# Performance work log

Measured on AMD Instinct MI355X. Metric: run time of the kernel, lower is better.

## Reference

```python
import jax, jax.numpy as jnp
import numpy as np

D_MODEL = 1024
NUM_HEADS = 16
B, S = 2, 2048


def setup_inputs() -> dict:
    key = jax.random.key(0)
    ks = jax.random.split(key, 11)
    scale = 1.0 / np.sqrt(D_MODEL)
    inp = {
        'q': jax.random.normal(ks[0], (B, S, D_MODEL), jnp.float32),
        'k': jax.random.normal(ks[1], (B, S, D_MODEL), jnp.float32),
        'v': jax.random.normal(ks[2], (B, S, D_MODEL), jnp.float32),
        'w_q': jax.random.normal(ks[3], (D_MODEL, D_MODEL), jnp.float32) * scale,
        'b_q': jax.random.normal(ks[4], (D_MODEL,), jnp.float32) * 0.01,
        'w_k': jax.random.normal(ks[5], (D_MODEL, D_MODEL), jnp.float32) * scale,
        'b_k': jax.random.normal(ks[6], (D_MODEL,), jnp.float32) * 0.01,
        'w_v': jax.random.normal(ks[7], (D_MODEL, D_MODEL), jnp.float32) * scale,
        'b_v': jax.random.normal(ks[8], (D_MODEL,), jnp.float32) * 0.01,
        'w_o': jax.random.normal(ks[9], (D_MODEL, D_MODEL), jnp.float32) * scale,
        'b_o': jax.random.normal(ks[10], (D_MODEL,), jnp.float32) * 0.01,
    }
    return inp


def reference(q, k, v, w_q, b_q, w_k, b_k, w_v, b_v, w_o, b_o):
    Bq, Sq, D = q.shape
    H = NUM_HEADS
    dh = D // H
    # projections (weights stored as [in, out])
    query = q @ w_q + b_q
    key = k @ w_k + b_k
    value = v @ w_v + b_v
    # [B, S, D] -> [B, H, S, dh]
    query = query.reshape(Bq, Sq, H, dh).transpose(0, 2, 1, 3)
    key = key.reshape(Bq, -1, H, dh).transpose(0, 2, 1, 3)
    value = value.reshape(Bq, -1, H, dh).transpose(0, 2, 1, 3)
    # NOTE: original module does NOT scale by 1/sqrt(dh)
    scores = jnp.einsum('bhqd,bhkd->bhqk', query, key)  # [B,H,S,S]
    causal_mask = jnp.triu(jnp.ones((Sq, Sq), dtype=bool), k=1)  # True above diag
    scores = jnp.where(causal_mask[None, None], -jnp.inf, scores)
    attn = jax.nn.softmax(scores, axis=-1)
    data = jnp.einsum('bhqk,bhkd->bhqd', attn, value)  # [B,H,S,dh]
    # FAITHFUL to original bug: transpose(0,1) then view(B, S, -1)
    data = data.transpose(1, 0, 2, 3).reshape(Bq, Sq, -1)  # [H,B,S,dh] -> [B,S,D]
    return data @ w_o + b_o
```

## Files before the change

### kernel.cpp

```cpp
#include <hip/hip_runtime.h>

typedef __fp16 f16;
typedef __fp16 f16x8 __attribute__((ext_vector_type(8)));
typedef __fp16 f16x4 __attribute__((ext_vector_type(4)));
typedef __fp16 f16x2 __attribute__((ext_vector_type(2)));
typedef float f32x4 __attribute__((ext_vector_type(4)));
typedef float f32x16 __attribute__((ext_vector_type(16)));

#define D_MODEL 1024
#define SEQ 2048
#define NH 16
#define MTOT 4096

typedef const __attribute__((address_space(1))) unsigned int* gp1_t;
typedef __attribute__((address_space(3))) unsigned int* lp3_t;

__device__ __forceinline__ void gload_lds16(const void* g, void* l) {
  __builtin_amdgcn_global_load_lds((gp1_t)g, (lp3_t)l, 16, 0, 0);
}

__device__ __forceinline__ int permrow(int r) {
  int bp = r >> 11, u = (r >> 7) & 15, t = r & 127;
  int g16 = (bp << 4) | u;
  return ((((g16 & 1) << 4) | (g16 >> 1)) << 7) + t;
}

__device__ __forceinline__ unsigned int pkrtz(float a, float b) {
  union { f16x2 h; unsigned int u; } z;
  z.h = __builtin_amdgcn_cvt_pkrtz(a, b);
  return z.u;
}

__global__ __launch_bounds__(256) void cvt_all(const float* __restrict__ q,
                                               const float* __restrict__ k,
                                               const float* __restrict__ v,
                                               const float* __restrict__ wq,
                                               const float* __restrict__ wk,
                                               const float* __restrict__ wv,
                                               const float* __restrict__ wo,
                                               f16* __restrict__ qkv16,
                                               f16* __restrict__ wT) {
  __shared__ float tl[64][65];
  int bid = blockIdx.x, tid = threadIdx.x;
  if (bid < 6144) {
    int i = bid * 256 + tid;
    const int NT = (MTOT * D_MODEL) / 8;
    const float* src;
    int t;
    if (i < NT) { src = q; t = i; }
    else if (i < 2 * NT) { src = k; t = i - NT; }
    else { src = v; t = i - 2 * NT; }
    const float4* s4 = (const float4*)src;
    float4 a = s4[2 * t], b = s4[2 * t + 1];
    f16x8 h;
    h[0] = (f16)a.x; h[1] = (f16)a.y; h[2] = (f16)a.z; h[3] = (f16)a.w;
    h[4] = (f16)b.x; h[5] = (f16)b.y; h[6] = (f16)b.z; h[7] = (f16)b.w;
    *(f16x8*)(qkv16 + (size_t)i * 8) = h;
  } else {
    int bb = bid - 6144;
    int mat = bb >> 8, tile = bb & 255;
    int tk = (tile >> 4) << 6, tn = (tile & 15) << 6;
    const float* W = mat == 0 ? wq : mat == 1 ? wk : mat == 2 ? wv : wo;
    int rr = tid >> 4, c4 = (tid & 15) << 2;
#pragma unroll
    for (int it = 0; it < 4; ++it) {
      const float* p = W + (size_t)(tk + it * 16 + rr) * D_MODEL + tn + c4;
      float4 val = *(const float4*)p;
      tl[it * 16 + rr][c4 + 0] = val.x;
      tl[it * 16 + rr][c4 + 1] = val.y;
      tl[it * 16 + rr][c4 + 2] = val.z;
      tl[it * 16 + rr][c4 + 3] = val.w;
    }
    __syncthreads();
    int n = tid & 63, kseg = (tid >> 6) << 4;
    f16x8 lo, hi;
#pragma unroll
    for (int j = 0; j < 8; ++j) lo[j] = (f16)tl[kseg + j][n];
#pragma unroll
    for (int j = 0; j < 8; ++j) hi[j] = (f16)tl[kseg + 8 + j][n];
    f16* d = wT + (size_t)mat * (D_MODEL * D_MODEL) + (size_t)(tn + n) * D_MODEL + tk + kseg;
    *(f16x8*)d = lo;
    *(f16x8*)(d + 8) = hi;
  }
}

#define SLOT_ELEM 16384
__global__ __launch_bounds__(512, 2) void gemm_qkv(const f16* __restrict__ q16,
                                                   const f16* __restrict__ k16,
                                                   const f16* __restrict__ v16,
                                                   const f16* __restrict__ wT,
                                                   const float* __restrict__ bq,
                                                   const float* __restrict__ bk,
                                                   const float* __restrict__ bv,
                                                   f16* __restrict__ Q16,
                                                   f16* __restrict__ K16,
                                                   f16* __restrict__ VT16) {
  extern __shared__ __attribute__((aligned(16))) f16 sm[];
  const int K = D_MODEL, N = D_MODEL;
  const size_t WEL = (size_t)D_MODEL * D_MODEL;
  int z = blockIdx.z;
  const f16* A = z == 0 ? q16 : z == 1 ? k16 : v16;
  const f16* BT = wT + (size_t)z * WEL;
  const float* bias = z == 0 ? bq : z == 1 ? bk : bv;

  int tid = threadIdx.x;
  int w = tid >> 6, lane = tid & 63;
  int g = lane >> 4, c = lane & 15;
  int wr = w >> 2, wc = w & 3;
  int m0 = blockIdx.x * 256, n0 = blockIdx.y * 256;
  f32x4 acc[8][4] = {};

  int sl0 = lane >> 3, s = lane & 7;
  int u = s ^ sl0;
  int rlow = u >> 2, gsl = u & 3;
  const f16* Agp = A + (size_t)(m0 + w * 32 + 2 * sl0 + rlow) * K + gsl * 8;
  const f16* Bgp = BT + (size_t)(n0 + w * 32 + 2 * sl0 + rlow) * K + gsl * 8;

#define STAGE_QKV(tt, bi)                                                    \
  {                                                                          \
    f16* dA = sm + (bi)*SLOT_ELEM + w * 1024;                                \
    f16* dB = dA + 8192;                                                     \
    const f16* sa = Agp + (size_t)(tt)*32;                                   \
    const f16* sb = Bgp + (size_t)(tt)*32;                                   \
    gload_lds16(sa, dA);                                                     \
    gload_lds16(sa + (size_t)16 * K, dA + 512);                              \
    gload_lds16(sb, dB);                                                     \
    gload_lds16(sb + (size_t)16 * K, dB + 512);                              \
  }

  STAGE_QKV(0, 0)
  STAGE_QKV(1, 1)
  STAGE_QKV(2, 2)

  const int NKT = K / 32;
  for (int t = 0; t < NKT; ++t) {
    if (t < NKT - 2) asm volatile("s_waitcnt vmcnt(8)" ::: "memory");
    else if (t == NKT - 2) asm volatile("s_waitcnt vmcnt(4)" ::: "memory");
    else asm volatile("s_waitcnt vmcnt(0)" ::: "memory");
    __builtin_amdgcn_sched_barrier(0);
    __builtin_amdgcn_s_barrier();
    __builtin_amdgcn_sched_barrier(0);
    if (t + 3 < NKT) STAGE_QKV(t + 3, (t + 3) & 3)

    const char* Ac = (const char*)(sm + (t & 3) * SLOT_ELEM);
    const char* Bc = Ac + 16384;
    f16x8 af[8], bf[4];
#pragma unroll
    for (int mi = 0; mi < 8; ++mi) {
      int row = wr * 128 + mi * 16 + c;
      int tb = (row >> 1) * 128 + (((((row & 1) << 2) | g) ^ ((row >> 1) & 7)) << 4);
      af[mi] = *(const f16x8*)(Ac + tb);
    }
#pragma unroll
    for (int ni = 0; ni < 4; ++ni) {
      int row = wc * 64 + ni * 16 + c;
      int tb = (row >> 1) * 128 + (((((row & 1) << 2) | g) ^ ((row >> 1) & 7)) << 4);
      bf[ni] = *(const f16x8*)(Bc + tb);
    }
    asm volatile("s_waitcnt lgkmcnt(0)" ::: "memory");
    __builtin_amdgcn_sched_barrier(0);
    __builtin_amdgcn_s_setprio(1);
#pragma unroll
    for (int mi = 0; mi < 8; ++mi)
#pragma unroll
      for (int ni = 0; ni < 4; ++ni)
        acc[mi][ni] = __builtin_amdgcn_mfma_f32_16x16x32_f16(af[mi], bf[ni], acc[mi][ni], 0, 0, 0);
    __builtin_amdgcn_s_setprio(0);
  }

  int rb = m0 + wr * 128;
  int cb = n0 + wc * 64;
  if (z < 2) {
    f16* O = z == 0 ? Q16 : K16;
#pragma unroll
    for (int m = 0; m < 8; ++m) {
      int row0 = rb + m * 16 + 4 * g;
#pragma unroll
      for (int n = 0; n < 4; ++n) {
        int col = cb + n * 16 + c;
        float bv2 = bias[col];
#pragma unroll
        for (int r = 0; r < 4; ++r) O[(size_t)(row0 + r) * N + col] = (f16)(acc[m][n][r] + bv2);
      }
    }
  } else {
    f16* O = VT16;
#pragma unroll
    for (int m = 0; m < 8; ++m) {
      int s0f = rb + m * 16 + 4 * g;
      int bb = s0f >> 11, ss = s0f & (SEQ - 1);
#pragma unroll
      for (int n = 0; n < 4; ++n) {
        int col = cb + n * 16 + c;
        float bv2 = bias[col];
        f16x4 hv;
#pragma unroll
        for (int r = 0; r < 4; ++r) hv[r] = (f16)(acc[m][n][r] + bv2);
        *(f16x4*)(O + ((size_t)(bb * NH + (col >> 6)) * 64 + (col & 63)) * SEQ + ss) = hv;
      }
    }
  }
}

__global__ __launch_bounds__(256, 2) void gemm_out(const f16* __restrict__ A,
                                                   const f16* __restrict__ BT,
                                                   const float* __restrict__ bias,
                                                   float* __restrict__ O) {
  const int K = D_MODEL, N = D_MODEL;
  __shared__ f16 As[64 * 64];
  __shared__ f16 Bs[128 * 64];
  int tid = threadIdx.x;
  int w = tid >> 6, lane = tid & 63;
  int g = lane >> 4, c = lane & 15;
  int wr = w >> 1, wc = w & 1;
  int m0 = blockIdx.x * 64, n0 = blockIdx.y * 128;
  f32x4 acc[2][4] = {};

  for (int kt = 0; kt < K; kt += 64) {
#pragma unroll
    for (int i = 0; i < 2; ++i) {
      int seg = w * 2 + i;
      int p = seg * 1024 + lane * 16;
      int row = p >> 7;
      int colb = (p & 127) ^ ((row & 7) << 4);
      int ae = kt + (colb >> 1);
      gload_lds16(A + (size_t)permrow(m0 + row) * K + ae, &As[seg * 512]);
    }
#pragma unroll
    for (int i = 0; i < 4; ++i) {
      int seg = w * 4 + i;
      int p = seg * 1024 + lane * 16;
      int row = p >> 7;
      int colb = (p & 127) ^ ((row & 7) << 4);
      int ae = kt + (colb >> 1);
      gload_lds16(BT + (size_t)(n0 + row) * K + ae, &Bs[seg * 512]);
    }
    __syncthreads();
    f16x8 af[2][2], bf[4][2];
#pragma unroll
    for (int m = 0; m < 2; ++m) {
#pragma unroll
      for (int kk = 0; kk < 2; ++kk) {
        int row = wr * 32 + m * 16 + c;
        int tb = (row * 128 + kk * 64 + g * 16) ^ ((row & 7) << 4);
        af[m][kk] = *(const f16x8*)((const char*)As + tb);
      }
    }
#pragma unroll
    for (int n = 0; n < 4; ++n) {
#pragma unroll
      for (int kk = 0; kk < 2; ++kk) {
        int row = wc * 64 + n * 16 + c;
        int tb = (row * 128 + kk * 64 + g * 16) ^ ((row & 7) << 4);
        bf[n][kk] = *(const f16x8*)((const char*)Bs + tb);
      }
    }
    __builtin_amdgcn_s_setprio(1);
#pragma unroll
    for (int m = 0; m < 2; ++m)
#pragma unroll
      for (int n = 0; n < 4; ++n)
#pragma unroll
        for (int kk = 0; kk < 2; ++kk)
          acc[m][n] = __builtin_amdgcn_mfma_f32_16x16x32_f16(af[m][kk], bf[n][kk], acc[m][n], 0, 0, 0);
    __builtin_amdgcn_s_setprio(0);
    __syncthreads();
  }

  int rb = m0 + wr * 32;
  int cb = n0 + wc * 64;
#pragma unroll
  for (int m = 0; m < 2; ++m) {
    int row0 = rb + m * 16 + 4 * g;
#pragma unroll
    for (int n = 0; n < 4; ++n) {
      int col = cb + n * 16 + c;
      float bv = bias[col];
#pragma unroll
      for (int r = 0; r < 4; ++r) O[(size_t)(row0 + r) * N + col] = acc[m][n][r] + bv;
    }
  }
}

#define THR2 11.5f
__global__ __launch_bounds__(256, 2) void attn_kernel(const f16* __restrict__ Q,
                                                      const f16* __restrict__ K,
                                                      const f16* __restrict__ VT,
                                                      f16* __restrict__ AO) {
  __shared__ __attribute__((aligned(16))) f16 Ksh[2][2][64 * 64];
  __shared__ __attribute__((aligned(16))) f16 Vsh[2][2][64 * 64];
  const int BUFO = 2 * 64 * 64;
  int tid = threadIdx.x;
  int w = tid >> 6, lane = tid & 63;
  int c = lane & 31, hi = lane >> 5;
  int qh = w & 1, par = w >> 1;
  int blk = blockIdx.x;
  int bh = blk & 31;
  int uu = blk >> 5;
  int cb = 31 - uu;
  int b = bh >> 4, h = bh & 15;
  int q0 = cb * 64 + qh * 32;
  const int NT = cb + 1;
  const size_t brow = (size_t)b * SEQ;
  const int hcol = h * 64;

  int sr = lane >> 3;
  int seo = ((lane & 7) ^ sr) << 3;
  const f16* Kgb = K + (size_t)(brow + qh * 32 + sr) * D_MODEL + hcol + seo;
  const f16* Vgb = VT + ((size_t)bh * 64 + qh * 32 + sr) * SEQ + seo;
  f16* Kshf = &Ksh[0][0][0];
  f16* Vshf = &Vsh[0][0][0];
  f16* KshW = Kshf + par * 4096 + qh * 32 * 64;
  f16* VshW = Vshf + par * 4096 + qh * 32 * 64;

  const f16 LOG2E = (f16)1.44269504f;
  f16x8 qf[4];
  const f16* Qp = Q + (size_t)(brow + q0 + c) * D_MODEL + hcol + 8 * hi;
#pragma unroll
  for (int kk = 0; kk < 4; ++kk) {
    qf[kk] = *(const f16x8*)(Qp + 16 * kk);
#pragma unroll
    for (int j = 0; j < 8; ++j) qf[kk][j] = (f16)(qf[kk][j] * LOG2E);
  }

  float m_st = -1e30f, l_st = 0.f;
  f32x16 o0 = {}, o1 = {};

  if (par < NT) {
    int kv = par * 64;
#pragma unroll
    for (int j = 0; j < 4; ++j) {
      gload_lds16(Kgb + (size_t)(kv + j * 8) * D_MODEL, KshW + (j * 8) * 64);
      gload_lds16(Vgb + (size_t)(j * 8) * SEQ + kv, VshW + (j * 8) * 64);
    }
  }
  __syncthreads();

  int rsw = (c & 7) << 4;
  int cur = 0;
  const int U = (NT + 1) >> 1;
  for (int u = 0; u < U; ++u) {
    int tpre = 2 * u + 2 + par;
    if (tpre < NT) {
      int kv = tpre * 64;
      f16* kd = KshW + (cur ^ 1) * BUFO;
      f16* vd = VshW + (cur ^ 1) * BUFO;
#pragma unroll
      for (int j = 0; j < 4; ++j) {
        gload_lds16(Kgb + (size_t)(kv + j * 8) * D_MODEL, kd + (j * 8) * 64);
        gload_lds16(Vgb + (size_t)(j * 8) * SEQ + kv, vd + (j * 8) * 64);
      }
    }
    int t = 2 * u + par;
    if (t < NT) {
      const char* Kb = (const char*)(Kshf + cur * BUFO + par * 4096);
      const char* Vb = (const char*)(Vshf + cur * BUFO + par * 4096);
      f16x8 kf[2][4];
#pragma unroll
      for (int ks = 0; ks < 2; ++ks)
#pragma unroll
        for (int kk = 0; kk < 4; ++kk)
          kf[ks][kk] = *(const f16x8*)(Kb + (((ks * 32 + c) * 128 + 32 * kk + 16 * hi) ^ rsw));
      f32x16 s0 = {}, s1 = {};
      __builtin_amdgcn_s_setprio(1);
#pragma unroll
      for (int kk = 0; kk < 4; ++kk) {
        s0 = __builtin_amdgcn_mfma_f32_32x32x16_f16(kf[0][kk], qf[kk], s0, 0, 0, 0);
        s1 = __builtin_amdgcn_mfma_f32_32x32x16_f16(kf[1][kk], qf[kk], s1, 0, 0, 0);
      }
      __builtin_amdgcn_s_setprio(0);
      f16x8 vf[2][4];
#pragma unroll
      for (int dt = 0; dt < 2; ++dt)
#pragma unroll
        for (int kk = 0; kk < 4; ++kk)
          vf[dt][kk] = *(const f16x8*)(Vb + (((dt * 32 + c) * 128 + 32 * kk + 16 * hi) ^ rsw));
      if (t == NT - 1) {
        int q = q0 + c;
        int kvb = t * 64 + 4 * hi;
#pragma unroll
        for (int r = 0; r < 16; ++r) {
          int kv = kvb + (r & 3) + 8 * (r >> 2);
          if (kv > q) s0[r] = -1e30f;
          if (kv + 32 > q) s1[r] = -1e30f;
        }
      }
      float t8[8];
#pragma unroll
      for (int r = 0; r < 8; ++r)
        t8[r] = fmaxf(fmaxf(s0[r], s0[r + 8]), fmaxf(s1[r], s1[r + 8]));
      float pm = fmaxf(fmaxf(fmaxf(t8[0], t8[1]), fmaxf(t8[2], t8[3])),
                       fmaxf(fmaxf(t8[4], t8[5]), fmaxf(t8[6], t8[7])));
      float mx = fmaxf(pm, __shfl_xor(pm, 32));
      if (__any(mx > m_st + THR2)) {
        float mnew = fmaxf(m_st, mx);
        float corr = __builtin_amdgcn_exp2f(m_st - mnew);
        l_st *= corr;
#pragma unroll
        for (int r = 0; r < 16; ++r) { o0[r] *= corr; o1[r] *= corr; }
        m_st = mnew;
      }
      float ts[16];
#pragma unroll
      for (int r = 0; r < 16; ++r) {
        float p0 = __builtin_amdgcn_exp2f(s0[r] - m_st);
        float p1 = __builtin_amdgcn_exp2f(s1[r] - m_st);
        s0[r] = p0; s1[r] = p1;
        ts[r] = p0 + p1;
      }
#pragma unroll
      for (int st = 8; st > 0; st >>= 1)
#pragma unroll
        for (int r = 0; r < st; ++r) ts[r] += ts[r + st];
      l_st += ts[0];
      union PU { unsigned int u[4]; f16x8 v; };
      PU pu[4];
#pragma unroll
      for (int kk = 0; kk < 4; ++kk) {
        int rb = 8 * (kk & 1);
        unsigned int la0, la1, lb0, lb1;
        if (kk < 2) {
          la0 = pkrtz(s0[rb + 0], s0[rb + 1]);
          la1 = pkrtz(s0[rb + 2], s0[rb + 3]);
          lb0 = pkrtz(s0[rb + 4], s0[rb + 5]);
          lb1 = pkrtz(s0[rb + 6], s0[rb + 7]);
        } else {
          la0 = pkrtz(s1[rb + 0], s1[rb + 1]);
          la1 = pkrtz(s1[rb + 2], s1[rb + 3]);
          lb0 = pkrtz(s1[rb + 4], s1[rb + 5]);
          lb1 = pkrtz(s1[rb + 6], s1[rb + 7]);
        }
        asm("v_permlane32_swap_b32 %0, %1" : "+v"(la0), "+v"(lb0));
        asm("v_permlane32_swap_b32 %0, %1" : "+v"(la1), "+v"(lb1));
        pu[kk].u[0] = la0; pu[kk].u[1] = la1; pu[kk].u[2] = lb0; pu[kk].u[3] = lb1;
      }
      __builtin_amdgcn_s_setprio(1);
#pragma unroll
      for (int kk = 0; kk < 4; ++kk) {
        o0 = __builtin_amdgcn_mfma_f32_32x32x16_f16(vf[0][kk], pu[kk].v, o0, 0, 0, 0);
        o1 = __builtin_amdgcn_mfma_f32_32x32x16_f16(vf[1][kk], pu[kk].v, o1, 0, 0, 0);
      }
      __builtin_amdgcn_s_setprio(0);
    }
    __syncthreads();
    cur ^= 1;
  }

  float* sc = (float*)Kshf;
  int mb = (qh * 64 + lane) * 34;
  if (par == 1) {
    sc[mb] = m_st;
    sc[mb + 1] = l_st;
#pragma unroll
    for (int r = 0; r < 16; ++r) { sc[mb + 2 + r] = o0[r]; sc[mb + 18 + r] = o1[r]; }
  }
  __syncthreads();
  if (par == 0) {
    float m1 = sc[mb], l1 = sc[mb + 1];
    float mm = fmaxf(m_st, m1);
    float c0 = __builtin_amdgcn_exp2f(m_st - mm);
    float c1 = __builtin_amdgcn_exp2f(m1 - mm);
    float l = l_st * c0 + l1 * c1;
#pragma unroll
    for (int r = 0; r < 16; ++r) {
      o0[r] = o0[r] * c0 + sc[mb + 2 + r] * c1;
      o1[r] = o1[r] * c0 + sc[mb + 18 + r] * c1;
    }
    float lt = l + __shfl_xor(l, 32);
    float linv = 1.0f / lt;
    f16* aoq = AO + ((size_t)bh * SEQ + q0 + c) * 64 + 4 * hi;
#pragma unroll
    for (int rq = 0; rq < 4; ++rq) {
      f16x4 h0, h1;
#pragma unroll
      for (int r = 0; r < 4; ++r) {
        h0[r] = (f16)(o0[4 * rq + r] * linv);
        h1[r] = (f16)(o1[4 * rq + r] * linv);
      }
      *(f16x4*)(aoq + 8 * rq) = h0;
      *(f16x4*)(aoq + 32 + 8 * rq) = h1;
    }
  }
}

extern "C" void kernel_launch(void* const* d_in, const int* in_sizes, int n_in,
                              void* d_out, int out_size, void* d_ws, size_t ws_size,
                              hipStream_t stream) {
  const float* q  = (const float*)d_in[0];
  const float* k  = (const float*)d_in[1];
  const float* v  = (const float*)d_in[2];
  const float* wq = (const float*)d_in[3];
  const float* bq = (const float*)d_in[4];
  const float* wk = (const float*)d_in[5];
  const float* bk = (const float*)d_in[6];
  const float* wv = (const float*)d_in[7];
  const float* bv = (const float*)d_in[8];
  const float* wo = (const float*)d_in[9];
  const float* bo = (const float*)d_in[10];

  const size_t TEN = (size_t)MTOT * D_MODEL;
  const size_t WEL = (size_t)D_MODEL * D_MODEL;
  f16* ws  = (f16*)d_ws;
  f16* q16 = ws;
  f16* k16 = q16 + TEN;
  f16* v16 = k16 + TEN;
  f16* wT  = v16 + TEN;
  f16* Q16 = wT + 4 * WEL;
  f16* K16 = Q16 + TEN;
  f16* VT16 = K16 + TEN;
  f16* AO  = q16;

  static bool attr_set = false;
  if (!attr_set) {
    hipFuncSetAttribute(reinterpret_cast<const void*>(&gemm_qkv),
                        hipFuncAttributeMaxDynamicSharedMemorySize, 131072);
    attr_set = true;
  }

  cvt_all<<<7168, 256, 0, stream>>>(q, k, v, wq, wk, wv, wo, q16, wT);
  gemm_qkv<<<dim3(16, 4, 3), 512, 131072, stream>>>(q16, k16, v16, wT, bq, bk, bv, Q16, K16, VT16);
  attn_kernel<<<1024, 256, 0, stream>>>(Q16, K16, VT16, AO);
  gemm_out<<<dim3(64, 8), 256, 0, stream>>>(AO, wT + 3 * WEL, bo, (float*)d_out);
}
```

Baseline: 109.2 us.

## Process both 32-row query halves per wave in attention, halving block threads

The attention kernel now uses 2 waves per block instead of 4. Each wave computes both 32-row query halves, so each K/V fragment read from shared memory feeds twice as many MFMAs. Each wave also issues twice as many global-to-LDS loads. This is meant to cut LDS read traffic and cross-wave duplication. In exchange each block has fewer waves and each wave needs more registers, which reduces latency hiding, and launch bounds change to (128,1).

```diff
diff --git a/kernel.cpp b/kernel.cpp
--- a/kernel.cpp
+++ b/kernel.cpp
@@ -283,7 +283,7 @@
 }
 
 #define THR2 11.5f
-__global__ __launch_bounds__(256, 2) void attn_kernel(const f16* __restrict__ Q,
+__global__ __launch_bounds__(128, 1) void attn_kernel(const f16* __restrict__ Q,
                                                       const f16* __restrict__ K,
                                                       const f16* __restrict__ VT,
                                                       f16* __restrict__ AO) {
@@ -291,45 +291,49 @@
   __shared__ __attribute__((aligned(16))) f16 Vsh[2][2][64 * 64];
   const int BUFO = 2 * 64 * 64;
   int tid = threadIdx.x;
-  int w = tid >> 6, lane = tid & 63;
+  int par = tid >> 6, lane = tid & 63;
   int c = lane & 31, hi = lane >> 5;
-  int qh = w & 1, par = w >> 1;
   int blk = blockIdx.x;
   int bh = blk & 31;
   int uu = blk >> 5;
   int cb = 31 - uu;
   int b = bh >> 4, h = bh & 15;
-  int q0 = cb * 64 + qh * 32;
+  int q0 = cb * 64;
   const int NT = cb + 1;
   const size_t brow = (size_t)b * SEQ;
   const int hcol = h * 64;
 
   int sr = lane >> 3;
   int seo = ((lane & 7) ^ sr) << 3;
-  const f16* Kgb = K + (size_t)(brow + qh * 32 + sr) * D_MODEL + hcol + seo;
-  const f16* Vgb = VT + ((size_t)bh * 64 + qh * 32 + sr) * SEQ + seo;
+  const f16* Kgb = K + (size_t)(brow + sr) * D_MODEL + hcol + seo;
+  const f16* Vgb = VT + ((size_t)bh * 64 + sr) * SEQ + seo;
   f16* Kshf = &Ksh[0][0][0];
   f16* Vshf = &Vsh[0][0][0];
-  f16* KshW = Kshf + par * 4096 + qh * 32 * 64;
-  f16* VshW = Vshf + par * 4096 + qh * 32 * 64;
+  f16* KshW = Kshf + par * 4096;
+  f16* VshW = Vshf + par * 4096;
 
   const f16 LOG2E = (f16)1.44269504f;
-  f16x8 qf[4];
-  const f16* Qp = Q + (size_t)(brow + q0 + c) * D_MODEL + hcol + 8 * hi;
+  f16x8 qfA[4], qfB[4];
+  const f16* QpA = Q + (size_t)(brow + q0 + c) * D_MODEL + hcol + 8 * hi;
+  const f16* QpB = Q + (size_t)(brow + q0 + 32 + c) * D_MODEL + hcol + 8 * hi;
 #pragma unroll
   for (int kk = 0; kk < 4; ++kk) {
-    qf[kk] = *(const f16x8*)(Qp + 16 * kk);
-#pragma unroll
-    for (int j = 0; j < 8; ++j) qf[kk][j] = (f16)(qf[kk][j] * LOG2E);
-  }
-
-  float m_st = -1e30f, l_st = 0.f;
-  f32x16 o0 = {}, o1 = {};
+    qfA[kk] = *(const f16x8*)(QpA + 16 * kk);
+    qfB[kk] = *(const f16x8*)(QpB + 16 * kk);
+#pragma unroll
+    for (int j = 0; j < 8; ++j) {
+      qfA[kk][j] = (f16)(qfA[kk][j] * LOG2E);
+      qfB[kk][j] = (f16)(qfB[kk][j] * LOG2E);
+    }
+  }
+
+  float mA = -1e30f, lA = 0.f, mB = -1e30f, lB = 0.f;
+  f32x16 oa0 = {}, oa1 = {}, ob0 = {}, ob1 = {};
 
   if (par < NT) {
     int kv = par * 64;
 #pragma unroll
-    for (int j = 0; j < 4; ++j) {
+    for (int j = 0; j < 8; ++j) {
       gload_lds16(Kgb + (size_t)(kv + j * 8) * D_MODEL, KshW + (j * 8) * 64);
       gload_lds16(Vgb + (size_t)(j * 8) * SEQ + kv, VshW + (j * 8) * 64);
     }
@@ -346,7 +350,7 @@
       f16* kd = KshW + (cur ^ 1) * BUFO;
       f16* vd = VshW + (cur ^ 1) * BUFO;
 #pragma unroll
-      for (int j = 0; j < 4; ++j) {
+      for (int j = 0; j < 8; ++j) {
         gload_lds16(Kgb + (size_t)(kv + j * 8) * D_MODEL, kd + (j * 8) * 64);
         gload_lds16(Vgb + (size_t)(j * 8) * SEQ + kv, vd + (j * 8) * 64);
       }
@@ -361,12 +365,14 @@
 #pragma unroll
         for (int kk = 0; kk < 4; ++kk)
           kf[ks][kk] = *(const f16x8*)(Kb + (((ks * 32 + c) * 128 + 32 * kk + 16 * hi) ^ rsw));
-      f32x16 s0 = {}, s1 = {};
+      f32x16 sa0 = {}, sa1 = {}, sb0 = {}, sb1 = {};
       __builtin_amdgcn_s_setprio(1);
 #pragma unroll
       for (int kk = 0; kk < 4; ++kk) {
-        s0 = __builtin_amdgcn_mfma_f32_32x32x16_f16(kf[0][kk], qf[kk], s0, 0, 0, 0);
-        s1 = __builtin_amdgcn_mfma_f32_32x32x16_f16(kf[1][kk], qf[kk], s1, 0, 0, 0);
+        sa0 = __builtin_amdgcn_mfma_f32_32x32x16_f16(kf[0][kk], qfA[kk], sa0, 0, 0, 0);
+        sa1 = __builtin_amdgcn_mfma_f32_32x32x16_f16(kf[1][kk], qfA[kk], sa1, 0, 0, 0);
+        sb0 = __builtin_amdgcn_mfma_f32_32x32x16_f16(kf[0][kk], qfB[kk], sb0, 0, 0, 0);
+        sb1 = __builtin_amdgcn_mfma_f32_32x32x16_f16(kf[1][kk], qfB[kk], sb1, 0, 0, 0);
       }
       __builtin_amdgcn_s_setprio(0);
       f16x8 vf[2][4];
@@ -376,109 +382,205 @@
         for (int kk = 0; kk < 4; ++kk)
           vf[dt][kk] = *(const f16x8*)(Vb + (((dt * 32 + c) * 128 + 32 * kk + 16 * hi) ^ rsw));
       if (t == NT - 1) {
-        int q = q0 + c;
+        int qA = q0 + c, qB = q0 + 32 + c;
         int kvb = t * 64 + 4 * hi;
 #pragma unroll
         for (int r = 0; r < 16; ++r) {
           int kv = kvb + (r & 3) + 8 * (r >> 2);
-          if (kv > q) s0[r] = -1e30f;
-          if (kv + 32 > q) s1[r] = -1e30f;
-        }
-      }
-      float t8[8];
-#pragma unroll
-      for (int r = 0; r < 8; ++r)
-        t8[r] = fmaxf(fmaxf(s0[r], s0[r + 8]), fmaxf(s1[r], s1[r + 8]));
-      float pm = fmaxf(fmaxf(fmaxf(t8[0], t8[1]), fmaxf(t8[2], t8[3])),
-                       fmaxf(fmaxf(t8[4], t8[5]), fmaxf(t8[6], t8[7])));
-      float mx = fmaxf(pm, __shfl_xor(pm, 32));
-      if (__any(mx > m_st + THR2)) {
-        float mnew = fmaxf(m_st, mx);
-        float corr = __builtin_amdgcn_exp2f(m_st - mnew);
-        l_st *= corr;
-#pragma unroll
-        for (int r = 0; r < 16; ++r) { o0[r] *= corr; o1[r] *= corr; }
-        m_st = mnew;
-      }
-      float ts[16];
-#pragma unroll
-      for (int r = 0; r < 16; ++r) {
-        float p0 = __builtin_amdgcn_exp2f(s0[r] - m_st);
-        float p1 = __builtin_amdgcn_exp2f(s1[r] - m_st);
-        s0[r] = p0; s1[r] = p1;
-        ts[r] = p0 + p1;
-      }
-#pragma unroll
-      for (int st = 8; st > 0; st >>= 1)
-#pragma unroll
-        for (int r = 0; r < st; ++r) ts[r] += ts[r + st];
-      l_st += ts[0];
+          if (kv > qA) sa0[r] = -1e30f;
+          if (kv + 32 > qA) sa1[r] = -1e30f;
+          if (kv > qB) sb0[r] = -1e30f;
+          if (kv + 32 > qB) sb1[r] = -1e30f;
+        }
+      }
+      {
+        float t8[8];
+#pragma unroll
+        for (int r = 0; r < 8; ++r)
+          t8[r] = fmaxf(fmaxf(sa0[r], sa0[r + 8]), fmaxf(sa1[r], sa1[r + 8]));
+        float pm = fmaxf(fmaxf(fmaxf(t8[0], t8[1]), fmaxf(t8[2], t8[3])),
+                         fmaxf(fmaxf(t8[4], t8[5]), fmaxf(t8[6], t8[7])));
+        float mx = fmaxf(pm, __shfl_xor(pm, 32));
+        if (__any(mx > mA + THR2)) {
+          float mnew = fmaxf(mA, mx);
+          float corr = __builtin_amdgcn_exp2f(mA - mnew);
+          lA *= corr;
+#pragma unroll
+          for (int r = 0; r < 16; ++r) { oa0[r] *= corr; oa1[r] *= corr; }
+          mA = mnew;
+        }
+        float ts[16];
+#pragma unroll
+        for (int r = 0; r < 16; ++r) {
+          float p0 = __builtin_amdgcn_exp2f(sa0[r] - mA);
+          float p1 = __builtin_amdgcn_exp2f(sa1[r] - mA);
+          sa0[r] = p0; sa1[r] = p1;
+          ts[r] = p0 + p1;
+        }
+#pragma unroll
+        for (int st = 8; st > 0; st >>= 1)
+#pragma unroll
+          for (int r = 0; r < st; ++r) ts[r] += ts[r + st];
+        lA += ts[0];
+      }
+      {
+        float t8[8];
+#pragma unroll
+        for (int r = 0; r < 8; ++r)
+          t8[r] = fmaxf(fmaxf(sb0[r], sb0[r + 8]), fmaxf(sb1[r], sb1[r + 8]));
+        float pm = fmaxf(fmaxf(fmaxf(t8[0], t8[1]), fmaxf(t8[2], t8[3])),
+                         fmaxf(fmaxf(t8[4], t8[5]), fmaxf(t8[6], t8[7])));
+        float mx = fmaxf(pm, __shfl_xor(pm, 32));
+        if (__any(mx > mB + THR2)) {
+          float mnew = fmaxf(mB, mx);
+          float corr = __builtin_amdgcn_exp2f(mB - mnew);
+          lB *= corr;
+#pragma unroll
+          for (int r = 0; r < 16; ++r) { ob0[r] *= corr; ob1[r] *= corr; }
+          mB = mnew;
+        }
+        float ts[16];
+#pragma unroll
+        for (int r = 0; r < 16; ++r) {
+          float p0 = __builtin_amdgcn_exp2f(sb0[r] - mB);
+          float p1 = __builtin_amdgcn_exp2f(sb1[r] - mB);
+          sb0[r] = p0; sb1[r] = p1;
+          ts[r] = p0 + p1;
+        }
+#pragma unroll
+        for (int st = 8; st > 0; st >>= 1)
+#pragma unroll
+          for (int r = 0; r < st; ++r) ts[r] += ts[r + st];
+        lB += ts[0];
+      }
       union PU { unsigned int u[4]; f16x8 v; };
-      PU pu[4];
-#pragma unroll
-      for (int kk = 0; kk < 4; ++kk) {
-        int rb = 8 * (kk & 1);
-        unsigned int la0, la1, lb0, lb1;
-        if (kk < 2) {
-          la0 = pkrtz(s0[rb + 0], s0[rb + 1]);
-          la1 = pkrtz(s0[rb + 2], s0[rb + 3]);
-          lb0 = pkrtz(s0[rb + 4], s0[rb + 5]);
-          lb1 = pkrtz(s0[rb + 6], s0[rb + 7]);
-        } else {
-          la0 = pkrtz(s1[rb + 0], s1[rb + 1]);
-          la1 = pkrtz(s1[rb + 2], s1[rb + 3]);
-          lb0 = pkrtz(s1[rb + 4], s1[rb + 5]);
-          lb1 = pkrtz(s1[rb + 6], s1[rb + 7]);
-        }
-        asm("v_permlane32_swap_b32 %0, %1" : "+v"(la0), "+v"(lb0));
-        asm("v_permlane32_swap_b32 %0, %1" : "+v"(la1), "+v"(lb1));
-        pu[kk].u[0] = la0; pu[kk].u[1] = la1; pu[kk].u[2] = lb0; pu[kk].u[3] = lb1;
-      }
-      __builtin_amdgcn_s_setprio(1);
-#pragma unroll
-      for (int kk = 0; kk < 4; ++kk) {
-        o0 = __builtin_amdgcn_mfma_f32_32x32x16_f16(vf[0][kk], pu[kk].v, o0, 0, 0, 0);
-        o1 = __builtin_amdgcn_mfma_f32_32x32x16_f16(vf[1][kk], pu[kk].v, o1, 0, 0, 0);
-      }
-      __builtin_amdgcn_s_setprio(0);
+      {
+        PU pu[4];
+#pragma unroll
+        for (int kk = 0; kk < 4; ++kk) {
+          int rb = 8 * (kk & 1);
+          unsigned int la0, la1, lb0, lb1;
+          if (kk < 2) {
+            la0 = pkrtz(sa0[rb + 0], sa0[rb + 1]);
+            la1 = pkrtz(sa0[rb + 2], sa0[rb + 3]);
+            lb0 = pkrtz(sa0[rb + 4], sa0[rb + 5]);
+            lb1 = pkrtz(sa0[rb + 6], sa0[rb + 7]);
+          } else {
+            la0 = pkrtz(sa1[rb + 0], sa1[rb + 1]);
+            la1 = pkrtz(sa1[rb + 2], sa1[rb + 3]);
+            lb0 = pkrtz(sa1[rb + 4], sa1[rb + 5]);
+            lb1 = pkrtz(sa1[rb + 6], sa1[rb + 7]);
+          }
+          asm("v_permlane32_swap_b32 %0, %1" : "+v"(la0), "+v"(lb0));
+          asm("v_permlane32_swap_b32 %0, %1" : "+v"(la1), "+v"(lb1));
+          pu[kk].u[0] = la0; pu[kk].u[1] = la1; pu[kk].u[2] = lb0; pu[kk].u[3] = lb1;
+        }
+        __builtin_amdgcn_s_setprio(1);
+#pragma unroll
+        for (int kk = 0; kk < 4; ++kk) {
+          oa0 = __builtin_amdgcn_mfma_f32_32x32x16_f16(vf[0][kk], pu[kk].v, oa0, 0, 0, 0);
+          oa1 = __builtin_amdgcn_mfma_f32_32x32x16_f16(vf[1][kk], pu[kk].v, oa1, 0, 0, 0);
+        }
+        __builtin_amdgcn_s_setprio(0);
+      }
+      {
+        PU pu[4];
+#pragma unroll
+        for (int kk = 0; kk < 4; ++kk) {
+          int rb = 8 * (kk & 1);
+          unsigned int la0, la1, lb0, lb1;
+          if (kk < 2) {
+            la0 = pkrtz(sb0[rb + 0], sb0[rb + 1]);
+            la1 = pkrtz(sb0[rb + 2], sb0[rb + 3]);
+            lb0 = pkrtz(sb0[rb + 4], sb0[rb + 5]);
+            lb1 = pkrtz(sb0[rb + 6], sb0[rb + 7]);
+          } else {
+            la0 = pkrtz(sb1[rb + 0], sb1[rb + 1]);
+            la1 = pkrtz(sb1[rb + 2], sb1[rb + 3]);
+            lb0 = pkrtz(sb1[rb + 4], sb1[rb + 5]);
+            lb1 = pkrtz(sb1[rb + 6], sb1[rb + 7]);
+          }
+          asm("v_permlane32_swap_b32 %0, %1" : "+v"(la0), "+v"(lb0));
+          asm("v_permlane32_swap_b32 %0, %1" : "+v"(la1), "+v"(lb1));
+          pu[kk].u[0] = la0; pu[kk].u[1] = la1; pu[kk].u[2] = lb0; pu[kk].u[3] = lb1;
+        }
+        __builtin_amdgcn_s_setprio(1);
+#pragma unroll
+        for (int kk = 0; kk < 4; ++kk) {
+          ob0 = __builtin_amdgcn_mfma_f32_32x32x16_f16(vf[0][kk], pu[kk].v, ob0, 0, 0, 0);
+          ob1 = __builtin_amdgcn_mfma_f32_32x32x16_f16(vf[1][kk], pu[kk].v, ob1, 0, 0, 0);
+        }
+        __builtin_amdgcn_s_setprio(0);
+      }
     }
     __syncthreads();
     cur ^= 1;
   }
 
   float* sc = (float*)Kshf;
-  int mb = (qh * 64 + lane) * 34;
+  int mbA = lane * 34;
+  int mbB = (64 + lane) * 34;
   if (par == 1) {
-    sc[mb] = m_st;
-    sc[mb + 1] = l_st;
-#pragma unroll
-    for (int r = 0; r < 16; ++r) { sc[mb + 2 + r] = o0[r]; sc[mb + 18 + r] = o1[r]; }
+    sc[mbA] = mA; sc[mbA + 1] = lA;
+#pragma unroll
+    for (int r = 0; r < 16; ++r) { sc[mbA + 2 + r] = oa0[r]; sc[mbA + 18 + r] = oa1[r]; }
+    sc[mbB] = mB; sc[mbB + 1] = lB;
+#pragma unroll
+    for (int r = 0; r < 16; ++r) { sc[mbB + 2 + r] = ob0[r]; sc[mbB + 18 + r] = ob1[r]; }
   }
   __syncthreads();
   if (par == 0) {
-    float m1 = sc[mb], l1 = sc[mb + 1];
-    float mm = fmaxf(m_st, m1);
-    float c0 = __builtin_amdgcn_exp2f(m_st - mm);
-    float c1 = __builtin_amdgcn_exp2f(m1 - mm);
-    float l = l_st * c0 + l1 * c1;
-#pragma unroll
-    for (int r = 0; r < 16; ++r) {
-      o0[r] = o0[r] * c0 + sc[mb + 2 + r] * c1;
-      o1[r] = o1[r] * c0 + sc[mb + 18 + r] * c1;
-    }
-    float lt = l + __shfl_xor(l, 32);
-    float linv = 1.0f / lt;
-    f16* aoq = AO + ((size_t)bh * SEQ + q0 + c) * 64 + 4 * hi;
-#pragma unroll
-    for (int rq = 0; rq < 4; ++rq) {
-      f16x4 h0, h1;
-#pragma unroll
-      for (int r = 0; r < 4; ++r) {
-        h0[r] = (f16)(o0[4 * rq + r] * linv);
-        h1[r] = (f16)(o1[4 * rq + r] * linv);
-      }
-      *(f16x4*)(aoq + 8 * rq) = h0;
-      *(f16x4*)(aoq + 32 + 8 * rq) = h1;
+    {
+      float m1 = sc[mbA], l1 = sc[mbA + 1];
+      float mm = fmaxf(mA, m1);
+      float c0 = __builtin_amdgcn_exp2f(mA - mm);
+      float c1 = __builtin_amdgcn_exp2f(m1 - mm);
+      float l = lA * c0 + l1 * c1;
+#pragma unroll
+      for (int r = 0; r < 16; ++r) {
+        oa0[r] = oa0[r] * c0 + sc[mbA + 2 + r] * c1;
+        oa1[r] = oa1[r] * c0 + sc[mbA + 18 + r] * c1;
+      }
+      float lt = l + __shfl_xor(l, 32);
+      float linv = 1.0f / lt;
+      f16* aoq = AO + ((size_t)bh * SEQ + q0 + c) * 64 + 4 * hi;
+#pragma unroll
+      for (int rq = 0; rq < 4; ++rq) {
+        f16x4 h0, h1;
+#pragma unroll
+        for (int r = 0; r < 4; ++r) {
+          h0[r] = (f16)(oa0[4 * rq + r] * linv);
+          h1[r] = (f16)(oa1[4 * rq + r] * linv);
+        }
+        *(f16x4*)(aoq + 8 * rq) = h0;
+        *(f16x4*)(aoq + 32 + 8 * rq) = h1;
+      }
+    }
+    {
+      float m1 = sc[mbB], l1 = sc[mbB + 1];
+      float mm = fmaxf(mB, m1);
+      float c0 = __builtin_amdgcn_exp2f(mB - mm);
+      float c1 = __builtin_amdgcn_exp2f(m1 - mm);
+      float l = lB * c0 + l1 * c1;
+#pragma unroll
+      for (int r = 0; r < 16; ++r) {
+        ob0[r] = ob0[r] * c0 + sc[mbB + 2 + r] * c1;
+        ob1[r] = ob1[r] * c0 + sc[mbB + 18 + r] * c1;
+      }
+      float lt = l + __shfl_xor(l, 32);
+      float linv = 1.0f / lt;
+      f16* aoq = AO + ((size_t)bh * SEQ + q0 + 32 + c) * 64 + 4 * hi;
+#pragma unroll
+      for (int rq = 0; rq < 4; ++rq) {
+        f16x4 h0, h1;
+#pragma unroll
+        for (int r = 0; r < 4; ++r) {
+          h0[r] = (f16)(ob0[4 * rq + r] * linv);
+          h1[r] = (f16)(ob1[4 * rq + r] * linv);
+        }
+        *(f16x4*)(aoq + 8 * rq) = h0;
+        *(f16x4*)(aoq + 32 + 8 * rq) = h1;
+      }
     }
   }
 }
@@ -519,6 +621,6 @@
 
   cvt_all<<<7168, 256, 0, stream>>>(q, k, v, wq, wk, wv, wo, q16, wT);
   gemm_qkv<<<dim3(16, 4, 3), 512, 131072, stream>>>(q16, k16, v16, wT, bq, bk, bv, Q16, K16, VT16);
-  attn_kernel<<<1024, 256, 0, stream>>>(Q16, K16, VT16, AO);
+  attn_kernel<<<1024, 128, 0, stream>>>(Q16, K16, VT16, AO);
   gemm_out<<<dim3(64, 8), 256, 0, stream>>>(AO, wT + 3 * WEL, bo, (float*)d_out);
 }
```

New measurement: 123.9 us. +13.4%, slower.
